# Kernel tuning notes

Hardware: AMD Instinct MI355X
Metric: run time of the kernel (lower is better)

The kernel has to match this reference:

```python
import jax, jax.numpy as jnp
import numpy as np

B, L, D, N, OUT, NL = 4, 1024, 512, 16, 512, 2  # batch, seq, channels, ssm state, output, layers


def setup_inputs() -> dict:
    key = jax.random.key(0)
    ks = jax.random.split(key, 8)
    sc = D ** -0.5
    return {
        "x": jax.random.normal(ks[0], (B, L, D), jnp.float32),
        # diagonal A: negative real part (real_random=False -> stable negative init)
        "A": -jax.random.uniform(ks[1], (NL, D, N), jnp.float32, 0.1, 1.0),
        "D_skip": jnp.ones((NL, D), jnp.float32),
        "WB": jax.random.normal(ks[2], (NL, D, N), jnp.float32) * sc,
        "bB": jnp.zeros((NL, N), jnp.float32),
        "WC": jax.random.normal(ks[3], (NL, D, N), jnp.float32) * sc,
        "bC": jnp.zeros((NL, N), jnp.float32),
        "Wdt": jax.random.normal(ks[4], (NL, D, D), jnp.float32) * sc,
        "bdt": jnp.full((NL, D), -4.0, jnp.float32),  # softplus(-4) ~ 0.018 -> small dt
        "Wlin": jax.random.normal(ks[5], (NL, D, D), jnp.float32) * sc,
        "blin": jnp.zeros((NL, D), jnp.float32),
        "Wdec": jax.random.normal(ks[6], (D, OUT), jnp.float32) * sc,
        "bdec": jnp.zeros((OUT,), jnp.float32),
    }


def _linear_scan(a, b):
    # first-order linear recurrence h_t = a_t * h_{t-1} + b_t via parallel scan
    def comb(c1, c2):
        a1, b1 = c1
        a2, b2 = c2
        return a1 * a2, a2 * b1 + b2
    return jax.lax.associative_scan(comb, (a, b), axis=1)[1]


def _forward(x, A, D_skip, WB, bB, WC, bC, Wdt, bdt, Wlin, blin, Wdec, bdec):
    y = x
    for i in range(NL):
        # selection mechanism: dt, B, C are input-dependent
        dt = jax.nn.softplus(jnp.einsum('bld,de->ble', y, Wdt[i]) + bdt[i])  # (B,L,D)
        Bm = jnp.einsum('bld,dn->bln', y, WB[i]) + bB[i]                      # (B,L,N)
        Cm = jnp.einsum('bld,dn->bln', y, WC[i]) + bC[i]                      # (B,L,N)
        # ZOH discretization of diagonal SSM
        a = jnp.exp(dt[..., None] * A[i])                                     # (B,L,D,N)
        b = (dt * y)[..., None] * Bm[:, :, None, :]                           # (B,L,D,N)
        h = _linear_scan(a, b)                                                # (B,L,D,N)
        out = jnp.einsum('bldn,bln->bld', h, Cm) + D_skip[i] * y
        y = jnp.maximum(out, 0.0)                                             # ReLU
        y = jnp.einsum('bld,de->ble', y, Wlin[i]) + blin[i]                   # per-layer Linear
    return jnp.einsum('bld,do->blo', y, Wdec) + bdec                          # decoder


def reference(x, A, D_skip, WB, bB, WC, bC, Wdt, bdt, Wlin, blin, Wdec, bdec):
    return _forward(x, A, D_skip, WB, bB, WC, bC, Wdt, bdt, Wlin, blin, Wdec, bdec)
```

## Files before the change

kernel.cpp:

```cpp
#include <hip/hip_runtime.h>

#define BQ 4
#define LQ 1024
#define DQ 512
#define NQ 16
#define MQ (BQ*LQ)
#define CHUNK 16
#define NCH (LQ/CHUNK)
#define KQ 512
#define NFUSE 576

typedef __bf16  bf16x8  __attribute__((ext_vector_type(8)));
typedef float   floatx4 __attribute__((ext_vector_type(4)));

__device__ __forceinline__ float softplus_f(float x) {
    return (x > 20.0f) ? x : log1pf(__expf(x));
}
__device__ __forceinline__ unsigned short f2b(float f) {
    union { float f; unsigned u; } x; x.f = f;
    unsigned r = x.u + 0x7fffu + ((x.u >> 16) & 1u);
    return (unsigned short)(r >> 16);
}
__device__ __forceinline__ float b2f(unsigned short u) {
    union { unsigned u; float f; } x; x.u = (unsigned)u << 16;
    return x.f;
}
__device__ __forceinline__ void load_lds16(const void* g, void* l) {
    __builtin_amdgcn_global_load_lds(
        (const __attribute__((address_space(1))) unsigned int*)g,
        (__attribute__((address_space(3))) unsigned int*)l, 16, 0, 0);
}

__device__ __forceinline__ void stage_tile(
    const unsigned short* g, unsigned short* lds, int wave, int lane)
{
    const int rsub = lane >> 3;
    const int gsrc = (lane & 7) ^ rsub;
    #pragma unroll
    for (int j = 0; j < 2; ++j) {
        int rbase = wave * 16 + j * 8;
        load_lds16(g + (size_t)(rbase + rsub) * KQ + gsrc * 8,
                   lds + (size_t)rbase * 64);
    }
}

__device__ __forceinline__ void gemm_db_core(
    const unsigned short* __restrict__ Abf,
    const unsigned short* __restrict__ Wt,
    int bm, int bn, int stag,
    unsigned short (*As)[64*64], unsigned short (*Bs)[64*64],
    floatx4 acc[2][2])
{
    const int lane = threadIdx.x & 63, wave = threadIdx.x >> 6;
    const int mw = (wave & 1) * 32, nw = (wave >> 1) * 32;
    const int r15 = lane & 15, q = lane >> 4;
    const int slot0 = q ^ (r15 & 7);

    #pragma unroll
    for (int i = 0; i < 2; ++i)
        #pragma unroll
        for (int j = 0; j < 2; ++j) acc[i][j] = (floatx4){0.f,0.f,0.f,0.f};

    const unsigned short* ga = Abf + (size_t)bm * KQ;
    const unsigned short* gb = Wt  + (size_t)bn * KQ;
    {
        int kt = (stag & 7) * 64;
        stage_tile(ga + kt, As[0], wave, lane);
        stage_tile(gb + kt, Bs[0], wave, lane);
    }

    #pragma unroll
    for (int it = 0; it < 8; ++it) {
        __syncthreads();
        if (it < 7) {
            int kt = ((it + 1 + stag) & 7) * 64;
            stage_tile(ga + kt, As[(it + 1) & 1], wave, lane);
            stage_tile(gb + kt, Bs[(it + 1) & 1], wave, lane);
        }
        const unsigned short* a = As[it & 1];
        const unsigned short* b = Bs[it & 1];
        #pragma unroll
        for (int ks = 0; ks < 2; ++ks) {
            int slot = slot0 ^ (ks * 4);
            bf16x8 af0 = *(const bf16x8*)&a[(mw      + r15) * 64 + slot * 8];
            bf16x8 af1 = *(const bf16x8*)&a[(mw + 16 + r15) * 64 + slot * 8];
            bf16x8 bf0 = *(const bf16x8*)&b[(nw      + r15) * 64 + slot * 8];
            bf16x8 bf1 = *(const bf16x8*)&b[(nw + 16 + r15) * 64 + slot * 8];
            acc[0][0] = __builtin_amdgcn_mfma_f32_16x16x32_bf16(af0, bf0, acc[0][0], 0,0,0);
            acc[1][0] = __builtin_amdgcn_mfma_f32_16x16x32_bf16(af1, bf0, acc[1][0], 0,0,0);
            acc[0][1] = __builtin_amdgcn_mfma_f32_16x16x32_bf16(af0, bf1, acc[0][1], 0,0,0);
            acc[1][1] = __builtin_amdgcn_mfma_f32_16x16x32_bf16(af1, bf1, acc[1][1], 0,0,0);
        }
    }
}

__device__ __forceinline__ void write_fused(
    floatx4 acc[2][2], int bm, int bn_local,
    const float* __restrict__ bias,
    unsigned short* __restrict__ dtb, float* __restrict__ Bm, float* __restrict__ Cm)
{
    const int lane = threadIdx.x & 63, wave = threadIdx.x >> 6;
    const int mw = (wave & 1) * 32, nw = (wave >> 1) * 32;
    const int col0 = lane & 15, rq = lane >> 4;
    #pragma unroll
    for (int nt = 0; nt < 2; ++nt) {
        int nb = bn_local + nw + nt * 16;
        int n  = nb + col0;
        if (nb >= 544) continue;
        float bv = bias[n];
        #pragma unroll
        for (int mt = 0; mt < 2; ++mt)
            #pragma unroll
            for (int r = 0; r < 4; ++r) {
                int m = bm + mw + mt * 16 + rq * 4 + r;
                float v = acc[mt][nt][r] + bv;
                if (nb < 512)      dtb[(size_t)m * DQ + n] = f2b(softplus_f(v));
                else if (nb < 528) Bm[(size_t)m * NQ + (n - 512)] = v;
                else               Cm[(size_t)m * NQ + (n - 528)] = v;
            }
    }
}

__global__ __launch_bounds__(256) void gemm_f0_compose(
    const unsigned short* __restrict__ y16,
    const unsigned short* __restrict__ Wf0, const float* __restrict__ bfused0,
    unsigned short* __restrict__ dtb0, float* __restrict__ Bm0, float* __restrict__ Cm0,
    const unsigned short* __restrict__ Wf1_t, const unsigned short* __restrict__ Wlin0_o,
    const unsigned short* __restrict__ Wdec_t, const unsigned short* __restrict__ Wlin1_o,
    const float* __restrict__ blin, const float* __restrict__ bdt,
    const float* __restrict__ bB, const float* __restrict__ bC,
    const float* __restrict__ bdec,
    unsigned short* __restrict__ Wcomb1, unsigned short* __restrict__ Wdec_comb,
    float* __restrict__ bcomb1, float* __restrict__ bdec_comb)
{
    __shared__ __align__(16) unsigned short As[2][64*64];
    __shared__ __align__(16) unsigned short Bs[2][64*64];
    const int bid = blockIdx.x, tid = threadIdx.x;
    if (bid < 576) {
        const int bm = (bid & 63) * 64, bn = (bid >> 6) * 64;
        floatx4 acc[2][2];
        gemm_db_core(y16, Wf0, bm, bn, bid, As, Bs, acc);
        write_fused(acc, bm, bn, bfused0, dtb0, Bm0, Cm0);
    } else if (bid < 712) {
        const unsigned short *Abf, *Wt; unsigned short* dst;
        int bm, bn;
        if (bid < 648) { int q = bid - 576; Abf = Wf1_t;  Wt = Wlin0_o; dst = Wcomb1;
                         bm = (q / 8) * 64; bn = (q % 8) * 64; }
        else           { int q = bid - 648; Abf = Wdec_t; Wt = Wlin1_o; dst = Wdec_comb;
                         bm = (q / 8) * 64; bn = (q % 8) * 64; }
        floatx4 acc[2][2];
        gemm_db_core(Abf, Wt, bm, bn, bid, As, Bs, acc);
        const int lane = tid & 63, wave = tid >> 6;
        const int mw = (wave & 1) * 32, nw = (wave >> 1) * 32;
        const int col0 = lane & 15, rq = lane >> 4;
        #pragma unroll
        for (int nt = 0; nt < 2; ++nt) {
            int n = bn + nw + nt * 16 + col0;
            #pragma unroll
            for (int mt = 0; mt < 2; ++mt)
                #pragma unroll
                for (int r = 0; r < 4; ++r) {
                    int m = bm + mw + mt * 16 + rq * 4 + r;
                    dst[(size_t)m * KQ + n] = f2b(acc[mt][nt][r]);
                }
        }
    } else {
        const int within = tid >> 3, part = tid & 7;
        float acc = 0.f;
        if (bid < 730) {
            int n = (bid - 712) * 32 + within;
            const unsigned short* wrow = Wf1_t + (size_t)n * KQ + part * 64;
            const float* bl = blin;
            #pragma unroll 8
            for (int j = 0; j < 64; ++j)
                acc = fmaf(bl[part * 64 + j], b2f(wrow[j]), acc);
            acc += __shfl_xor(acc, 1);
            acc += __shfl_xor(acc, 2);
            acc += __shfl_xor(acc, 4);
            if (part == 0) {
                float base;
                if (n < 512)      base = bdt[DQ + n];
                else if (n < 528) base = bB[NQ + (n - 512)];
                else if (n < 544) base = bC[NQ + (n - 528)];
                else              base = 0.f;
                bcomb1[n] = acc + base;
            }
        } else {
            int n = (bid - 730) * 32 + within;
            const unsigned short* wrow = Wdec_t + (size_t)n * KQ + part * 64;
            const float* bl = blin + DQ;
            #pragma unroll 8
            for (int j = 0; j < 64; ++j)
                acc = fmaf(bl[part * 64 + j], b2f(wrow[j]), acc);
            acc += __shfl_xor(acc, 1);
            acc += __shfl_xor(acc, 2);
            acc += __shfl_xor(acc, 4);
            if (part == 0) bdec_comb[n] = acc + bdec[n];
        }
    }
}

__global__ __launch_bounds__(256) void gemm_pair(
    const unsigned short* __restrict__ Abf,
    const unsigned short* __restrict__ Wt_lin0,
    const unsigned short* __restrict__ Wcomb1,
    const float* __restrict__ blin0, const float* __restrict__ bcomb1,
    unsigned short* __restrict__ y16b,
    unsigned short* __restrict__ dtb1, float* __restrict__ Bm1, float* __restrict__ Cm1)
{
    __shared__ __align__(16) unsigned short As[2][64*64];
    __shared__ __align__(16) unsigned short Bs[2][64*64];
    const int bm = blockIdx.x * 64;
    const int tile = blockIdx.y;
    const int stag = blockIdx.x + blockIdx.y;
    floatx4 acc[2][2];
    if (tile < 8) {
        const int bn = tile * 64;
        gemm_db_core(Abf, Wt_lin0, bm, bn, stag, As, Bs, acc);
        const int lane = threadIdx.x & 63, wave = threadIdx.x >> 6;
        const int mw = (wave & 1) * 32, nw = (wave >> 1) * 32;
        const int col0 = lane & 15, rq = lane >> 4;
        #pragma unroll
        for (int nt = 0; nt < 2; ++nt) {
            int n = bn + nw + nt * 16 + col0;
            float bv = blin0[n];
            #pragma unroll
            for (int mt = 0; mt < 2; ++mt)
                #pragma unroll
                for (int r = 0; r < 4; ++r) {
                    int m = bm + mw + mt * 16 + rq * 4 + r;
                    y16b[(size_t)m * DQ + n] = f2b(acc[mt][nt][r] + bv);
                }
        }
    } else {
        const int bn = (tile - 8) * 64;
        gemm_db_core(Abf, Wcomb1, bm, bn, stag, As, Bs, acc);
        write_fused(acc, bm, bn, bcomb1, dtb1, Bm1, Cm1);
    }
}

__global__ __launch_bounds__(256) void gemm_final(
    const unsigned short* __restrict__ Abf,
    const unsigned short* __restrict__ Wt,
    const float* __restrict__ bias,
    float* __restrict__ out)
{
    __shared__ __align__(16) unsigned short As[2][64*64];
    __shared__ __align__(16) unsigned short Bs[2][64*64];
    const int bm = blockIdx.x * 64, bn = blockIdx.y * 64;
    floatx4 acc[2][2];
    gemm_db_core(Abf, Wt, bm, bn, blockIdx.x + blockIdx.y, As, Bs, acc);
    const int lane = threadIdx.x & 63, wave = threadIdx.x >> 6;
    const int mw = (wave & 1) * 32, nw = (wave >> 1) * 32;
    const int col0 = lane & 15, rq = lane >> 4;
    #pragma unroll
    for (int nt = 0; nt < 2; ++nt) {
        int n = bn + nw + nt * 16 + col0;
        float bv = bias[n];
        #pragma unroll
        for (int mt = 0; mt < 2; ++mt)
            #pragma unroll
            for (int r = 0; r < 4; ++r) {
                int m = bm + mw + mt * 16 + rq * 4 + r;
                out[(size_t)m * DQ + n] = acc[mt][nt][r] + bv;
            }
    }
}

__global__ __launch_bounds__(256) void prep_all(
    const float* __restrict__ Wdt, const float* __restrict__ Wlin,
    const float* __restrict__ Wdec,
    const float* __restrict__ WB, const float* __restrict__ WC,
    const float* __restrict__ x,
    const float* __restrict__ bdt, const float* __restrict__ bB,
    const float* __restrict__ bC,
    unsigned short* __restrict__ Wf0, unsigned short* __restrict__ Wf1,
    unsigned short* __restrict__ Wt_lin0, unsigned short* __restrict__ Wdec_t,
    unsigned short* __restrict__ Wlin0_o, unsigned short* __restrict__ Wlin1_o,
    unsigned short* __restrict__ y16, float* __restrict__ bfused0)
{
    const int bid = blockIdx.x, tid = threadIdx.x;
    if (bid < 1024) {
        __shared__ float tile[32][33];
        int mat = bid >> 8, t = bid & 255;
        const float* src; unsigned short* dst;
        switch (mat) {
            case 0:  src = Wdt;                  dst = Wf0;     break;
            case 1:  src = Wdt + (size_t)KQ*KQ;  dst = Wf1;     break;
            case 2:  src = Wlin;                 dst = Wt_lin0; break;
            default: src = Wdec;                 dst = Wdec_t;  break;
        }
        int bx = (t & 15) * 32, by = (t >> 4) * 32;
        int tx = tid & 31, ty = tid >> 5;
        #pragma unroll
        for (int i = 0; i < 32; i += 8)
            tile[ty + i][tx] = src[(size_t)(bx + ty + i) * KQ + by + tx];
        __syncthreads();
        #pragma unroll
        for (int i = 0; i < 32; i += 8)
            dst[(size_t)(by + ty + i) * KQ + bx + tx] = f2b(tile[tx][ty + i]);
    } else if (bid < 1536) {
        int q = bid - 1024;
        const float* src = (q < 256) ? Wlin : Wlin + (size_t)KQ*KQ;
        unsigned short* dst = (q < 256) ? Wlin0_o : Wlin1_o;
        size_t i = ((size_t)(q & 255) * 256 + tid) * 4;
        float4 v = *(const float4*)(src + i);
        ushort4 o;
        o.x = f2b(v.x); o.y = f2b(v.y); o.z = f2b(v.z); o.w = f2b(v.w);
        *(ushort4*)(dst + i) = o;
    } else if (bid < 1664) {
        int job = bid - 1536;
        int layer = job >> 6, r = job & 63;
        unsigned short* dst = (layer ? Wf1 : Wf0) + (size_t)(512 + r) * KQ;
        const float* src = nullptr;
        int n = 0;
        if (r < 16)      { src = WB + (size_t)layer * DQ * NQ; n = r; }
        else if (r < 32) { src = WC + (size_t)layer * DQ * NQ; n = r - 16; }
        for (int k = tid; k < KQ; k += 256)
            dst[k] = src ? f2b(src[(size_t)k * NQ + n]) : (unsigned short)0;
    } else if (bid < 3712) {
        size_t i = ((size_t)(bid - 1664) * 256 + tid) * 4;
        float4 v = *(const float4*)(x + i);
        ushort4 o;
        o.x = f2b(v.x); o.y = f2b(v.y); o.z = f2b(v.z); o.w = f2b(v.w);
        *(ushort4*)(y16 + i) = o;
    } else {
        int i = (bid - 3712) * 256 + tid;
        if (i < 512)      bfused0[i] = bdt[i];
        else if (i < 528) bfused0[i] = bB[i - 512];
        else if (i < 544) bfused0[i] = bC[i - 528];
        else if (i < 576) bfused0[i] = 0.f;
    }
}

__global__ __launch_bounds__(256) void scan_phase1(
    const unsigned short* __restrict__ dt, const unsigned short* __restrict__ y,
    const float* __restrict__ Bm, const float* __restrict__ A,
    unsigned short* __restrict__ ap, unsigned short* __restrict__ hf)
{
    int idx  = blockIdx.x;
    int dblk = idx & 1;
    int c    = (idx >> 1) & (NCH - 1);
    int b    = idx >> 7;
    int d    = dblk * 256 + threadIdx.x;

    float Ad[NQ];
    const float* Aptr = A + (size_t)d * NQ;
    #pragma unroll
    for (int n = 0; n < NQ; ++n) Ad[n] = Aptr[n];

    float h[NQ], prod[NQ];
    #pragma unroll
    for (int n = 0; n < NQ; ++n) { h[n] = 0.f; prod[n] = 1.f; }

    int t0 = c * CHUNK;
    const unsigned short* dtp = dt + ((size_t)b*LQ + t0) * DQ + d;
    const unsigned short* yp  = y  + ((size_t)b*LQ + t0) * DQ + d;
    const float* bp  = Bm + ((size_t)b*LQ + t0) * NQ;

    #pragma unroll 4
    for (int t = 0; t < CHUNK; ++t) {
        float dtv = b2f(dtp[(size_t)t * DQ]);
        float yv  = b2f(yp[(size_t)t * DQ]);
        float dty = dtv * yv;
        #pragma unroll
        for (int n = 0; n < NQ; ++n) {
            float a = __expf(dtv * Ad[n]);
            prod[n] *= a;
            h[n] = fmaf(a, h[n], dty * bp[t*NQ + n]);
        }
    }
    size_t base = ((size_t)(b*NCH + c) * DQ + d) * NQ;
    #pragma unroll
    for (int n = 0; n < NQ; n += 4) {
        ushort4 pa, ph;
        pa.x = f2b(prod[n]);   pa.y = f2b(prod[n+1]);
        pa.z = f2b(prod[n+2]); pa.w = f2b(prod[n+3]);
        ph.x = f2b(h[n]);   ph.y = f2b(h[n+1]);
        ph.z = f2b(h[n+2]); ph.w = f2b(h[n+3]);
        *(ushort4*)(ap + base + n) = pa;
        *(ushort4*)(hf + base + n) = ph;
    }
}

__global__ __launch_bounds__(256) void scan_phase2(
    unsigned short* ap, const unsigned short* __restrict__ hf)
{
    int g = blockIdx.x * 256 + threadIdx.x;
    int n = g & (NQ - 1);
    int d = (g >> 4) & (DQ - 1);
    int b = g >> 13;
    const size_t stride = (size_t)DQ * NQ;
    size_t base = ((size_t)b * NCH * DQ + d) * NQ + n;
    float h = 0.f;
    for (int c0 = 0; c0 < NCH; c0 += 8) {
        float a[8], f[8];
        #pragma unroll
        for (int j = 0; j < 8; ++j) {
            size_t idx = base + (size_t)(c0 + j) * stride;
            a[j] = b2f(ap[idx]);
            f[j] = b2f(hf[idx]);
        }
        #pragma unroll
        for (int j = 0; j < 8; ++j) {
            size_t idx = base + (size_t)(c0 + j) * stride;
            ap[idx] = f2b(h);
            h = fmaf(a[j], h, f[j]);
        }
    }
}

__global__ __launch_bounds__(256) void scan_phase3(
    const unsigned short* __restrict__ dt, const unsigned short* __restrict__ y,
    const float* __restrict__ Bm, const float* __restrict__ Cm,
    const float* __restrict__ A, const float* __restrict__ Dsk,
    const unsigned short* __restrict__ hi, unsigned short* __restrict__ yact)
{
    int idx  = blockIdx.x;
    int dblk = idx & 1;
    int c    = (idx >> 1) & (NCH - 1);
    int b    = idx >> 7;
    int d    = dblk * 256 + threadIdx.x;

    float Ad[NQ];
    const float* Aptr = A + (size_t)d * NQ;
    #pragma unroll
    for (int n = 0; n < NQ; ++n) Ad[n] = Aptr[n];

    float h[NQ];
    size_t base = ((size_t)(b*NCH + c) * DQ + d) * NQ;
    #pragma unroll
    for (int n = 0; n < NQ; n += 4) {
        ushort4 v = *(const ushort4*)(hi + base + n);
        h[n] = b2f(v.x); h[n+1] = b2f(v.y); h[n+2] = b2f(v.z); h[n+3] = b2f(v.w);
    }
    float dskip = Dsk[d];

    int t0 = c * CHUNK;
    const unsigned short* dtp = dt + ((size_t)b*LQ + t0) * DQ + d;
    const unsigned short* yp  = y  + ((size_t)b*LQ + t0) * DQ + d;
    const float* bp  = Bm + ((size_t)b*LQ + t0) * NQ;
    const float* cp  = Cm + ((size_t)b*LQ + t0) * NQ;
    unsigned short* op = yact + ((size_t)b*LQ + t0) * DQ + d;

    #pragma unroll 4
    for (int t = 0; t < CHUNK; ++t) {
        float dtv = b2f(dtp[(size_t)t * DQ]);
        float yv  = b2f(yp[(size_t)t * DQ]);
        float dty = dtv * yv;
        float acc = 0.f;
        #pragma unroll
        for (int n = 0; n < NQ; ++n) {
            float a = __expf(dtv * Ad[n]);
            h[n] = fmaf(a, h[n], dty * bp[t*NQ + n]);
            acc = fmaf(h[n], cp[t*NQ + n], acc);
        }
        float v = acc + dskip * yv;
        op[(size_t)t * DQ] = f2b(fmaxf(v, 0.f));
    }
}

extern "C" void kernel_launch(void* const* d_in, const int* in_sizes, int n_in,
                              void* d_out, int out_size, void* d_ws, size_t ws_size,
                              hipStream_t stream)
{
    const float* x    = (const float*)d_in[0];
    const float* A    = (const float*)d_in[1];
    const float* Dsk  = (const float*)d_in[2];
    const float* WB   = (const float*)d_in[3];
    const float* bB   = (const float*)d_in[4];
    const float* WC   = (const float*)d_in[5];
    const float* bC   = (const float*)d_in[6];
    const float* Wdt  = (const float*)d_in[7];
    const float* bdt  = (const float*)d_in[8];
    const float* Wlin = (const float*)d_in[9];
    const float* blin = (const float*)d_in[10];
    const float* Wdec = (const float*)d_in[11];
    const float* bdec = (const float*)d_in[12];
    float* out = (float*)d_out;

    char* cur = (char*)d_ws;
    float* Bm0  = (float*)cur;  cur += (size_t)MQ*NQ*4;
    float* Cm0  = (float*)cur;  cur += (size_t)MQ*NQ*4;
    float* Bm1  = (float*)cur;  cur += (size_t)MQ*NQ*4;
    float* Cm1  = (float*)cur;  cur += (size_t)MQ*NQ*4;
    unsigned short* ap = (unsigned short*)cur; cur += (size_t)BQ*NCH*DQ*NQ*2;
    unsigned short* hf = (unsigned short*)cur; cur += (size_t)BQ*NCH*DQ*NQ*2;
    unsigned short* y16    = (unsigned short*)cur; cur += (size_t)MQ*DQ*2;
    unsigned short* y16b   = (unsigned short*)cur; cur += (size_t)MQ*DQ*2;
    unsigned short* dtb0   = (unsigned short*)cur; cur += (size_t)MQ*DQ*2;
    unsigned short* dtb1   = (unsigned short*)cur; cur += (size_t)MQ*DQ*2;
    unsigned short* yact   = (unsigned short*)cur; cur += (size_t)MQ*DQ*2;
    unsigned short* Wf0    = (unsigned short*)cur; cur += (size_t)NFUSE*KQ*2;
    unsigned short* Wf1    = (unsigned short*)cur; cur += (size_t)NFUSE*KQ*2;
    unsigned short* Wt_lin0 = (unsigned short*)cur; cur += (size_t)KQ*KQ*2;
    unsigned short* Wdec_t  = (unsigned short*)cur; cur += (size_t)KQ*KQ*2;
    unsigned short* Wlin0_o = (unsigned short*)cur; cur += (size_t)KQ*KQ*2;
    unsigned short* Wlin1_o = (unsigned short*)cur; cur += (size_t)KQ*KQ*2;
    unsigned short* Wcomb1  = (unsigned short*)cur; cur += (size_t)NFUSE*KQ*2;
    unsigned short* Wdec_comb = (unsigned short*)cur; cur += (size_t)KQ*KQ*2;
    float* bfused0   = (float*)cur;  cur += NFUSE*4;
    float* bcomb1    = (float*)cur;  cur += NFUSE*4;
    float* bdec_comb = (float*)cur;  cur += DQ*4;

    dim3 blk(256);

    prep_all<<<dim3(3715), blk, 0, stream>>>(
        Wdt, Wlin, Wdec, WB, WC, x, bdt, bB, bC,
        Wf0, Wf1, Wt_lin0, Wdec_t, Wlin0_o, Wlin1_o, y16, bfused0);

    gemm_f0_compose<<<dim3(746), blk, 0, stream>>>(
        y16, Wf0, bfused0, dtb0, Bm0, Cm0,
        Wf1, Wlin0_o, Wdec_t, Wlin1_o,
        blin, bdt, bB, bC, bdec,
        Wcomb1, Wdec_comb, bcomb1, bdec_comb);

    scan_phase1<<<dim3(BQ*NCH*2), blk, 0, stream>>>(dtb0, y16, Bm0, A, ap, hf);
    scan_phase2<<<dim3(BQ*DQ*NQ/256), blk, 0, stream>>>(ap, hf);
    scan_phase3<<<dim3(BQ*NCH*2), blk, 0, stream>>>(
        dtb0, y16, Bm0, Cm0, A, Dsk, ap, yact);

    gemm_pair<<<dim3(MQ/64, 17), blk, 0, stream>>>(
        yact, Wt_lin0, Wcomb1, blin, bcomb1, y16b, dtb1, Bm1, Cm1);

    scan_phase1<<<dim3(BQ*NCH*2), blk, 0, stream>>>(
        dtb1, y16b, Bm1, A + (size_t)DQ*NQ, ap, hf);
    scan_phase2<<<dim3(BQ*DQ*NQ/256), blk, 0, stream>>>(ap, hf);
    scan_phase3<<<dim3(BQ*NCH*2), blk, 0, stream>>>(
        dtb1, y16b, Bm1, Cm1, A + (size_t)DQ*NQ, Dsk + DQ, ap, yact);

    gemm_final<<<dim3(MQ/64, 8), blk, 0, stream>>>(
        yact, Wdec_comb, bdec_comb, out);
}
```

Before: 181.4 us.

## Rewrite final GEMM with per-wave private LDS quad-buffered async pipeline

Replaces the shared double-buffered block GEMM in the decoder projection with a per-wave scheme. Each wave stages its own 32x32 A/B slices into a private 4-deep LDS ring via direct global-to-LDS loads, using swizzled addressing and explicit vmcnt waits, so no block-level barriers are needed. This targets barrier stalls and improves load/MFMA overlap, at the cost of 64KB LDS per block, which limits occupancy. It also loses the data sharing between waves that the block-level tiling provided.

```diff
diff --git a/kernel.cpp b/kernel.cpp
--- a/kernel.cpp
+++ b/kernel.cpp
@@ -239,31 +239,70 @@
     }
 }
 
+__device__ __forceinline__ void wp_stage(
+    const unsigned short* gA, const unsigned short* gB,
+    unsigned short* buf, int kt, int row16, int gsrc)
+{
+    load_lds16(gA + (size_t)row16        * KQ + kt + gsrc * 8, buf);
+    load_lds16(gA + (size_t)(16 + row16) * KQ + kt + gsrc * 8, buf + 512);
+    load_lds16(gB + (size_t)row16        * KQ + kt + gsrc * 8, buf + 1024);
+    load_lds16(gB + (size_t)(16 + row16) * KQ + kt + gsrc * 8, buf + 1536);
+}
+
 __global__ __launch_bounds__(256) void gemm_final(
     const unsigned short* __restrict__ Abf,
     const unsigned short* __restrict__ Wt,
     const float* __restrict__ bias,
     float* __restrict__ out)
 {
-    __shared__ __align__(16) unsigned short As[2][64*64];
-    __shared__ __align__(16) unsigned short Bs[2][64*64];
-    const int bm = blockIdx.x * 64, bn = blockIdx.y * 64;
-    floatx4 acc[2][2];
-    gemm_db_core(Abf, Wt, bm, bn, blockIdx.x + blockIdx.y, As, Bs, acc);
+    __shared__ __align__(16) unsigned short WP[32768];
     const int lane = threadIdx.x & 63, wave = threadIdx.x >> 6;
     const int mw = (wave & 1) * 32, nw = (wave >> 1) * 32;
-    const int col0 = lane & 15, rq = lane >> 4;
-    #pragma unroll
-    for (int nt = 0; nt < 2; ++nt) {
-        int n = bn + nw + nt * 16 + col0;
-        float bv = bias[n];
-        #pragma unroll
-        for (int mt = 0; mt < 2; ++mt)
-            #pragma unroll
-            for (int r = 0; r < 4; ++r) {
-                int m = bm + mw + mt * 16 + rq * 4 + r;
-                out[(size_t)m * DQ + n] = acc[mt][nt][r] + bv;
-            }
+    const int bm = blockIdx.x * 64 + mw, bn = blockIdx.y * 64 + nw;
+    unsigned short* my = WP + wave * 8192;
+    const unsigned short* gA = Abf + (size_t)bm * KQ;
+    const unsigned short* gB = Wt  + (size_t)bn * KQ;
+    const int r15 = lane & 15, q = lane >> 4;
+    const int row16 = lane >> 2, gsrc = (lane & 3) ^ (row16 & 3);
+    const int sw = r15 & 3;
+
+    float bv0 = bias[bn + r15];
+    float bv1 = bias[bn + 16 + r15];
+    __builtin_amdgcn_s_waitcnt(0xF70);
+
+    floatx4 a00 = {0.f,0.f,0.f,0.f}, a01 = a00, a10 = a00, a11 = a00;
+
+    wp_stage(gA, gB, my + 0 * 2048,  0, row16, gsrc);
+    wp_stage(gA, gB, my + 1 * 2048, 32, row16, gsrc);
+    wp_stage(gA, gB, my + 2 * 2048, 64, row16, gsrc);
+
+    #pragma unroll
+    for (int i = 0; i < 16; ++i) {
+        if (i < 13)
+            wp_stage(gA, gB, my + ((i + 3) & 3) * 2048, (i + 3) * 32, row16, gsrc);
+        if (i <= 12)      __builtin_amdgcn_s_waitcnt(0xF70 | 12);
+        else if (i == 13) __builtin_amdgcn_s_waitcnt(0xF70 | 8);
+        else if (i == 14) __builtin_amdgcn_s_waitcnt(0xF70 | 4);
+        else              __builtin_amdgcn_s_waitcnt(0xF70);
+        __builtin_amdgcn_sched_barrier(0);
+        const unsigned short* bp_ = my + (i & 3) * 2048;
+        bf16x8 af0 = *(const bf16x8*)(bp_ +        (      r15) * 32 + (q ^ sw) * 8);
+        bf16x8 af1 = *(const bf16x8*)(bp_ +        (16 +  r15) * 32 + (q ^ sw) * 8);
+        bf16x8 bf0 = *(const bf16x8*)(bp_ + 1024 + (      r15) * 32 + (q ^ sw) * 8);
+        bf16x8 bf1 = *(const bf16x8*)(bp_ + 1024 + (16 +  r15) * 32 + (q ^ sw) * 8);
+        a00 = __builtin_amdgcn_mfma_f32_16x16x32_bf16(af0, bf0, a00, 0,0,0);
+        a10 = __builtin_amdgcn_mfma_f32_16x16x32_bf16(af1, bf0, a10, 0,0,0);
+        a01 = __builtin_amdgcn_mfma_f32_16x16x32_bf16(af0, bf1, a01, 0,0,0);
+        a11 = __builtin_amdgcn_mfma_f32_16x16x32_bf16(af1, bf1, a11, 0,0,0);
+    }
+
+    #pragma unroll
+    for (int r = 0; r < 4; ++r) {
+        int m0 = bm + q * 4 + r, m1 = bm + 16 + q * 4 + r;
+        out[(size_t)m0 * DQ + bn + r15]      = a00[r] + bv0;
+        out[(size_t)m1 * DQ + bn + r15]      = a10[r] + bv0;
+        out[(size_t)m0 * DQ + bn + 16 + r15] = a01[r] + bv1;
+        out[(size_t)m1 * DQ + bn + 16 + r15] = a11[r] + bv1;
     }
 }
 
```

Result: no change. 179.5 us (median of 2 runs) (-1.0%).
